# Kernel optimization log

Hardware: AMD Instinct MI355X
Metric: run time of the kernel (lower is better)

## Reference

```python
import jax, jax.numpy as jnp
import numpy as np

K = 3          # up_k
EPS = 1e-8
BN_EPS = 1e-5
NEG_SLOPE = 0.2


def _knn(dense_xyz, sparse_xyz, k):
    # dense_xyz: (B,3,N), sparse_xyz: (B,3,S) -> squared dists (B,N,k), idx (B,N,k)
    inner = jnp.einsum('bcn,bcs->bns', dense_xyz, sparse_xyz)
    n2 = jnp.sum(dense_xyz * dense_xyz, axis=1)   # (B,N)
    s2 = jnp.sum(sparse_xyz * sparse_xyz, axis=1)  # (B,S)
    d2 = n2[:, :, None] + s2[:, None, :] - 2.0 * inner  # (B,N,S)
    d2 = jnp.maximum(d2, 0.0)
    neg_d, idx = jax.lax.top_k(-d2, k)  # k smallest distances
    return -neg_d, idx


def setup_inputs() -> dict:
    key = jax.random.key(0)
    ks = jax.random.split(key, 7)
    B, N, S = 4, 16384, 4096
    Cd, Cs = 128, 256           # dense / sparse feature channels (Cd + Cs = 3*v_dense)
    Co = 128                    # v_dense
    return {
        'dense_points_xyz': jax.random.normal(ks[0], (B, 3, N), jnp.float32),
        'sparse_points_xyz': jax.random.normal(ks[1], (B, 3, S), jnp.float32),
        'dense_points_data': jax.random.normal(ks[2], (B, Cd, N), jnp.float32),
        'sparse_points_data': jax.random.normal(ks[3], (B, Cs, S), jnp.float32),
        'conv_w': jax.random.normal(ks[4], (Co, Cd + Cs), jnp.float32) * (1.0 / np.sqrt(Cd + Cs)),
        'bn_gamma': jnp.ones((Co,), jnp.float32),
        'bn_beta': jnp.zeros((Co,), jnp.float32),
    }


def reference(dense_points_xyz, sparse_points_xyz, dense_points_data,
              sparse_points_data, conv_w, bn_gamma, bn_beta):
    # ---- interpolate: KNN + inverse-distance weighted sum ----
    d, idx = _knn(dense_points_xyz, sparse_points_xyz, K)   # (B,N,K) each
    # gather sparse features: (B,Cs,S), idx (B,N,K) -> (B,Cs,N,K)
    neighbors = jax.vmap(lambda sd, ix: sd[:, ix])(sparse_points_data, idx)
    w = 1.0 / (d + EPS)
    w = w / jnp.sum(w, axis=-1, keepdims=True)              # (B,N,K)
    interp = jnp.sum(neighbors * w[:, None, :, :], axis=-1)  # (B,Cs,N)

    # ---- concat + 1x1 conv + BatchNorm (training-mode batch stats) + LeakyReLU ----
    x = jnp.concatenate([dense_points_data, interp], axis=1)  # (B, 3*v_dense, N)
    y = jnp.einsum('oc,bcn->bon', conv_w, x)                  # (B, v_dense, N)
    mean = jnp.mean(y, axis=(0, 2), keepdims=True)
    var = jnp.var(y, axis=(0, 2), keepdims=True)
    y = (y - mean) * jax.lax.rsqrt(var + BN_EPS)
    y = y * bn_gamma[None, :, None] + bn_beta[None, :, None]
    y = jnp.where(y >= 0, y, NEG_SLOPE * y)
    return y, dense_points_xyz
```

## Files before the change

kernel.cpp:

```cpp
#include <hip/hip_runtime.h>

constexpr int B  = 4;
constexpr int N  = 16384;
constexpr int S  = 4096;
constexpr int CD = 128;
constexpr int CS = 256;
constexpr int CO = 128;
constexpr int CIN = CD + CS;

constexpr int NC = 8;
constexpr int CH = S / NC;
constexpr int P  = 2;

__device__ __forceinline__ double pack_key(float dist, unsigned sg) {
  return __longlong_as_double(
      (long long)(__double_as_longlong((double)dist) | (unsigned long long)sg));
}

__device__ __forceinline__ void insert3(double& k0, double& k1, double& k2,
                                        double x) {
  const double m0 = fmax(k0, x);
  const double m1 = fmax(k1, x);
  k0 = fmin(k0, x);
  k1 = fmin(k1, m0);
  k2 = fmin(k2, m1);
}

__global__ __launch_bounds__(256) void knn_chunk_kernel(
    const float* __restrict__ dxyz, const float* __restrict__ sxyz,
    double* __restrict__ ckey) {
  __shared__ float4 sp[CH];
  const int b = blockIdx.z;
  const int c = blockIdx.y;
  const int nbase = blockIdx.x * (256 * P);
  const int t = threadIdx.x;

  const float* sb = sxyz + b * 3 * S + c * CH;
  for (int j = t; j < CH; j += 256)
    sp[j] = make_float4(sb[j], sb[S + j], sb[2 * S + j], 0.f);
  __syncthreads();

  float bx[P], by[P], bz[P];
  double k0[P], k1[P], k2[P];
  #pragma unroll
  for (int p = 0; p < P; ++p) {
    const int n = nbase + p * 256 + t;
    bx[p] = dxyz[b * 3 * N + n];
    by[p] = dxyz[b * 3 * N + N + n];
    bz[p] = dxyz[b * 3 * N + 2 * N + n];
    k0[p] = k1[p] = k2[p] = 1e300;
  }

  #pragma unroll 4
  for (int j = 0; j < CH; ++j) {
    const float4 q = sp[j];
    const unsigned sg = (unsigned)(c * CH + j);
    #pragma unroll
    for (int p = 0; p < P; ++p) {
      const float ex = bx[p] - q.x, ey = by[p] - q.y, ez = bz[p] - q.z;
      const float dist = fmaf(ex, ex, fmaf(ey, ey, ez * ez));
      insert3(k0[p], k1[p], k2[p], pack_key(dist, sg));
    }
  }

  #pragma unroll
  for (int p = 0; p < P; ++p) {
    const int n = nbase + p * 256 + t;
    const size_t base = (((size_t)c * B + b) * N + n) * 3;
    ckey[base + 0] = k0[p];
    ckey[base + 1] = k1[p];
    ckey[base + 2] = k2[p];
  }
}

__global__ __launch_bounds__(256) void knn_merge_kernel(
    const double* __restrict__ ckey, float* __restrict__ wgt,
    int* __restrict__ idx) {
  const int gid = blockIdx.x * 256 + threadIdx.x;
  double k0 = 1e300, k1 = 1e300, k2 = 1e300;
  #pragma unroll
  for (int c = 0; c < NC; ++c) {
    const size_t base = ((size_t)c * B * N + gid) * 3;
    insert3(k0, k1, k2, ckey[base + 0]);
    insert3(k0, k1, k2, ckey[base + 1]);
    insert3(k0, k1, k2, ckey[base + 2]);
  }
  const long long b0 = __double_as_longlong(k0);
  const long long b1 = __double_as_longlong(k1);
  const long long b2 = __double_as_longlong(k2);
  const float d0 = (float)__longlong_as_double(b0 & ~0xFFFll);
  const float d1 = (float)__longlong_as_double(b1 & ~0xFFFll);
  const float d2 = (float)__longlong_as_double(b2 & ~0xFFFll);
  const float w0 = 1.f / (d0 + 1e-8f);
  const float w1 = 1.f / (d1 + 1e-8f);
  const float w2 = 1.f / (d2 + 1e-8f);
  const float inv = 1.f / (w0 + w1 + w2);
  const size_t base = (size_t)gid * 3;
  wgt[base + 0] = w0 * inv;
  wgt[base + 1] = w1 * inv;
  wgt[base + 2] = w2 * inv;
  idx[base + 0] = (int)(b0 & 0xFFFll);
  idx[base + 1] = (int)(b1 & 0xFFFll);
  idx[base + 2] = (int)(b2 & 0xFFFll);
}

__global__ __launch_bounds__(256) void wtrans_kernel(
    const float* __restrict__ cw, float* __restrict__ wt) {
  const int i = blockIdx.x * 256 + threadIdx.x;
  const int o = i / CIN;
  const int c = i - o * CIN;
  wt[c * CO + o] = cw[i];
}

__global__ __launch_bounds__(64) void zproj_kernel(
    const float* __restrict__ sdata, const float* __restrict__ wt,
    float* __restrict__ Z) {
  const int b = blockIdx.z;
  const int og = blockIdx.y;
  const int s = blockIdx.x * 64 + threadIdx.x;
  const float* __restrict__ xp = sdata + b * CS * S + s;
  const float* __restrict__ wp = wt + CD * CO + og * 16;

  float acc[16];
  #pragma unroll
  for (int i = 0; i < 16; ++i) acc[i] = 0.f;

  #pragma unroll 4
  for (int c = 0; c < CS; ++c) {
    const float xv = xp[c * S];
    #pragma unroll
    for (int i = 0; i < 16; ++i)
      acc[i] = fmaf(wp[c * CO + i], xv, acc[i]);
  }

  float4* zp = reinterpret_cast<float4*>(Z + (b * S + s) * CO + og * 16);
  #pragma unroll
  for (int i = 0; i < 4; ++i)
    zp[i] = make_float4(acc[4*i+0], acc[4*i+1], acc[4*i+2], acc[4*i+3]);
}

__global__ __launch_bounds__(256) void ygemm_kernel(
    const float* __restrict__ ddata, const float* __restrict__ cw,
    const float* __restrict__ Z, const float* __restrict__ wgt,
    const int* __restrict__ idx, float* __restrict__ y) {
  const int b = blockIdx.y;
  const int n = blockIdx.x * 64 + (threadIdx.x & 63);
  const int rg = __builtin_amdgcn_readfirstlane(threadIdx.x >> 6);
  const float* __restrict__ xp = ddata + b * CD * N + n;
  const float* __restrict__ wp = cw + rg * 32 * CIN;

  float acc[32];
  #pragma unroll
  for (int i = 0; i < 32; ++i) acc[i] = 0.f;

  #pragma unroll 4
  for (int c = 0; c < CD; ++c) {
    const float xv = xp[c * N];
    #pragma unroll
    for (int i = 0; i < 32; ++i)
      acc[i] = fmaf(wp[i * CIN + c], xv, acc[i]);
  }

  const int pb = (b * N + n) * 3;
  #pragma unroll
  for (int k = 0; k < 3; ++k) {
    const float wk = wgt[pb + k];
    const int ik = idx[pb + k];
    const float4* zp =
        reinterpret_cast<const float4*>(Z + (b * S + ik) * CO + rg * 32);
    #pragma unroll
    for (int i = 0; i < 8; ++i) {
      float4 zv = zp[i];
      acc[4*i+0] = fmaf(wk, zv.x, acc[4*i+0]);
      acc[4*i+1] = fmaf(wk, zv.y, acc[4*i+1]);
      acc[4*i+2] = fmaf(wk, zv.z, acc[4*i+2]);
      acc[4*i+3] = fmaf(wk, zv.w, acc[4*i+3]);
    }
  }

  float* yp = y + b * CO * N + (rg * 32) * N + n;
  #pragma unroll
  for (int i = 0; i < 32; ++i) yp[i * N] = acc[i];
}

__global__ __launch_bounds__(256) void stats_kernel(
    const float* __restrict__ y, float* __restrict__ stats) {
  const int o = blockIdx.x;
  const int b = blockIdx.y;
  const float4* yp = reinterpret_cast<const float4*>(y + (b * CO + o) * N);
  float s = 0.f, sq = 0.f;
  for (int j = threadIdx.x; j < N / 4; j += 256) {
    float4 v = yp[j];
    s  += v.x + v.y + v.z + v.w;
    sq += v.x * v.x + v.y * v.y + v.z * v.z + v.w * v.w;
  }
  __shared__ float ls[256];
  __shared__ float lq[256];
  ls[threadIdx.x] = s;
  lq[threadIdx.x] = sq;
  __syncthreads();
  for (int st = 128; st > 0; st >>= 1) {
    if (threadIdx.x < (unsigned)st) {
      ls[threadIdx.x] += ls[threadIdx.x + st];
      lq[threadIdx.x] += lq[threadIdx.x + st];
    }
    __syncthreads();
  }
  if (threadIdx.x == 0) {
    atomicAdd(&stats[o], ls[0]);
    atomicAdd(&stats[CO + o], lq[0]);
  }
}

__global__ void scaleshift_kernel(const float* __restrict__ stats,
                                  const float* __restrict__ gamma,
                                  const float* __restrict__ beta,
                                  float* __restrict__ ss) {
  const int o = threadIdx.x;
  const float invc = 1.f / (float)(B * N);
  const float m = stats[o] * invc;
  float v = stats[CO + o] * invc - m * m;
  v = fmaxf(v, 0.f);
  const float sc = gamma[o] / sqrtf(v + 1e-5f);
  ss[o] = sc;
  ss[CO + o] = beta[o] - m * sc;
}

__global__ __launch_bounds__(256) void norm_kernel(float* __restrict__ y,
                                                   const float* __restrict__ ss) {
  const int i = blockIdx.x * 256 + threadIdx.x;
  const int o = (i >> 12) & (CO - 1);
  const float sc = ss[o];
  const float sh = ss[CO + o];
  float4* yp = reinterpret_cast<float4*>(y);
  float4 v = yp[i];
  float t;
  t = fmaf(v.x, sc, sh); v.x = fmaxf(t, 0.2f * t);
  t = fmaf(v.y, sc, sh); v.y = fmaxf(t, 0.2f * t);
  t = fmaf(v.z, sc, sh); v.z = fmaxf(t, 0.2f * t);
  t = fmaf(v.w, sc, sh); v.w = fmaxf(t, 0.2f * t);
  yp[i] = v;
}

extern "C" void kernel_launch(void* const* d_in, const int* in_sizes, int n_in,
                              void* d_out, int out_size, void* d_ws, size_t ws_size,
                              hipStream_t stream) {
  const float* dxyz  = (const float*)d_in[0];
  const float* sxyz  = (const float*)d_in[1];
  const float* ddata = (const float*)d_in[2];
  const float* sdata = (const float*)d_in[3];
  const float* cw    = (const float*)d_in[4];
  const float* gamma = (const float*)d_in[5];
  const float* beta  = (const float*)d_in[6];
  float* out = (float*)d_out;

  char* wsb = (char*)d_ws;
  float*  wgt  = (float*) (wsb);
  int*    idx  = (int*)   (wsb + 786432);
  double* ckey = (double*)(wsb + 1572864);
  float*  Z    = (float*) (wsb + 1572864);
  float*  wt   = (float*) (wsb + 9961472);
  float*  stats= (float*) (wsb + 14155776);
  float*  ss   = (float*) (wsb + 14156800);

  hipMemsetAsync(stats, 0, 2 * CO * sizeof(float), stream);

  knn_chunk_kernel<<<dim3(N / (256 * P), NC, B), 256, 0, stream>>>(dxyz, sxyz, ckey);
  knn_merge_kernel<<<dim3(B * N / 256), 256, 0, stream>>>(ckey, wgt, idx);
  wtrans_kernel   <<<dim3(CO * CIN / 256), 256, 0, stream>>>(cw, wt);
  zproj_kernel    <<<dim3(S / 64, CO / 16, B), 64, 0, stream>>>(sdata, wt, Z);
  ygemm_kernel    <<<dim3(N / 64, B), 256, 0, stream>>>(ddata, cw, Z, wgt, idx, out);
  stats_kernel    <<<dim3(CO, B), 256, 0, stream>>>(out, stats);
  scaleshift_kernel<<<1, 128, 0, stream>>>(stats, gamma, beta, ss);
  norm_kernel     <<<(B * CO * N / 4) / 256, 256, 0, stream>>>(out, ss);

  hipMemcpyAsync(out + (size_t)B * CO * N, dxyz, (size_t)B * 3 * N * sizeof(float),
                 hipMemcpyDeviceToDevice, stream);
}
```

Baseline: 243.2 us.

## Two-pass float KNN with expanded distance and recomputed weights in merge

The KNN chunk kernel now uses the expanded form s2 - 2*x·s, precomputed per sparse point in shared memory. A first pass keeps the top-3 in plain floats using min/med3, and a second pass builds packed double keys only for candidates at or below the third-best threshold. Packing is sign-aware because the partial distance can be negative, and the merge kernel recomputes the true squared distances from the coordinates to form the weights. The chunk count is halved, so ckey traffic drops but there are fewer blocks. The cost is scanning each chunk twice, and ties may order differently from the reference.

```diff
diff --git a/kernel.cpp b/kernel.cpp
--- a/kernel.cpp
+++ b/kernel.cpp
@@ -8,14 +8,9 @@
 constexpr int CO = 128;
 constexpr int CIN = CD + CS;
 
-constexpr int NC = 8;
+constexpr int NC = 4;
 constexpr int CH = S / NC;
 constexpr int P  = 2;
-
-__device__ __forceinline__ double pack_key(float dist, unsigned sg) {
-  return __longlong_as_double(
-      (long long)(__double_as_longlong((double)dist) | (unsigned long long)sg));
-}
 
 __device__ __forceinline__ void insert3(double& k0, double& k1, double& k2,
                                         double x) {
@@ -24,6 +19,17 @@
   k0 = fmin(k0, x);
   k1 = fmin(k1, m0);
   k2 = fmin(k2, m1);
+}
+
+__device__ __forceinline__ double pack_key(float t, unsigned sg) {
+  const unsigned sga = (t < 0.f) ? (0xFFFu ^ sg) : sg;
+  return __longlong_as_double(__double_as_longlong((double)t) |
+                              (unsigned long long)sga);
+}
+__device__ __forceinline__ int unpack_idx(double k) {
+  const long long bits = __double_as_longlong(k);
+  const int low = (int)(bits & 0xFFFll);
+  return (bits < 0) ? (0xFFF ^ low) : low;
 }
 
 __global__ __launch_bounds__(256) void knn_chunk_kernel(
@@ -36,30 +42,50 @@
   const int t = threadIdx.x;
 
   const float* sb = sxyz + b * 3 * S + c * CH;
-  for (int j = t; j < CH; j += 256)
-    sp[j] = make_float4(sb[j], sb[S + j], sb[2 * S + j], 0.f);
+  for (int j = t; j < CH; j += 256) {
+    const float sx = sb[j], sy = sb[S + j], sz = sb[2 * S + j];
+    sp[j] = make_float4(-2.f * sx, -2.f * sy, -2.f * sz,
+                        fmaf(sx, sx, fmaf(sy, sy, sz * sz)));
+  }
   __syncthreads();
 
   float bx[P], by[P], bz[P];
-  double k0[P], k1[P], k2[P];
+  float d0[P], d1[P], d2[P];
   #pragma unroll
   for (int p = 0; p < P; ++p) {
     const int n = nbase + p * 256 + t;
     bx[p] = dxyz[b * 3 * N + n];
     by[p] = dxyz[b * 3 * N + N + n];
     bz[p] = dxyz[b * 3 * N + 2 * N + n];
-    k0[p] = k1[p] = k2[p] = 1e300;
+    d0[p] = d1[p] = d2[p] = 1e30f;
   }
 
   #pragma unroll 4
   for (int j = 0; j < CH; ++j) {
     const float4 q = sp[j];
+    #pragma unroll
+    for (int p = 0; p < P; ++p) {
+      const float x = fmaf(q.x, bx[p], fmaf(q.y, by[p], fmaf(q.z, bz[p], q.w)));
+      d2[p] = fminf(fmaxf(x, d1[p]), d2[p]);
+      d1[p] = __builtin_amdgcn_fmed3f(x, d0[p], d1[p]);
+      d0[p] = fminf(x, d0[p]);
+    }
+  }
+
+  double k0[P], k1[P], k2[P];
+  #pragma unroll
+  for (int p = 0; p < P; ++p) { k0[p] = k1[p] = k2[p] = 1e300; }
+
+  #pragma unroll 2
+  for (int j = 0; j < CH; ++j) {
+    const float4 q = sp[j];
     const unsigned sg = (unsigned)(c * CH + j);
     #pragma unroll
     for (int p = 0; p < P; ++p) {
-      const float ex = bx[p] - q.x, ey = by[p] - q.y, ez = bz[p] - q.z;
-      const float dist = fmaf(ex, ex, fmaf(ey, ey, ez * ez));
-      insert3(k0[p], k1[p], k2[p], pack_key(dist, sg));
+      const float x = fmaf(q.x, bx[p], fmaf(q.y, by[p], fmaf(q.z, bz[p], q.w)));
+      if (x <= d2[p]) {
+        insert3(k0[p], k1[p], k2[p], pack_key(x, sg));
+      }
     }
   }
 
@@ -74,9 +100,12 @@
 }
 
 __global__ __launch_bounds__(256) void knn_merge_kernel(
-    const double* __restrict__ ckey, float* __restrict__ wgt,
+    const double* __restrict__ ckey, const float* __restrict__ dxyz,
+    const float* __restrict__ sxyz, float* __restrict__ wgt,
     int* __restrict__ idx) {
   const int gid = blockIdx.x * 256 + threadIdx.x;
+  const int b = gid >> 14;
+  const int n = gid & (N - 1);
   double k0 = 1e300, k1 = 1e300, k2 = 1e300;
   #pragma unroll
   for (int c = 0; c < NC; ++c) {
@@ -85,23 +114,34 @@
     insert3(k0, k1, k2, ckey[base + 1]);
     insert3(k0, k1, k2, ckey[base + 2]);
   }
-  const long long b0 = __double_as_longlong(k0);
-  const long long b1 = __double_as_longlong(k1);
-  const long long b2 = __double_as_longlong(k2);
-  const float d0 = (float)__longlong_as_double(b0 & ~0xFFFll);
-  const float d1 = (float)__longlong_as_double(b1 & ~0xFFFll);
-  const float d2 = (float)__longlong_as_double(b2 & ~0xFFFll);
-  const float w0 = 1.f / (d0 + 1e-8f);
-  const float w1 = 1.f / (d1 + 1e-8f);
-  const float w2 = 1.f / (d2 + 1e-8f);
-  const float inv = 1.f / (w0 + w1 + w2);
+  int ii[3];
+  ii[0] = unpack_idx(k0);
+  ii[1] = unpack_idx(k1);
+  ii[2] = unpack_idx(k2);
+
+  const float bx = dxyz[b * 3 * N + n];
+  const float by = dxyz[b * 3 * N + N + n];
+  const float bz = dxyz[b * 3 * N + 2 * N + n];
+  const float n2 = bx * bx + by * by + bz * bz;
+  float w[3];
+  #pragma unroll
+  for (int k = 0; k < 3; ++k) {
+    const float sx = sxyz[b * 3 * S + ii[k]];
+    const float sy = sxyz[b * 3 * S + S + ii[k]];
+    const float sz = sxyz[b * 3 * S + 2 * S + ii[k]];
+    const float s2 = sx * sx + sy * sy + sz * sz;
+    const float inner = bx * sx + by * sy + bz * sz;
+    const float d = fmaxf((n2 + s2) - 2.f * inner, 0.f);
+    w[k] = 1.f / (d + 1e-8f);
+  }
+  const float inv = 1.f / (w[0] + w[1] + w[2]);
   const size_t base = (size_t)gid * 3;
-  wgt[base + 0] = w0 * inv;
-  wgt[base + 1] = w1 * inv;
-  wgt[base + 2] = w2 * inv;
-  idx[base + 0] = (int)(b0 & 0xFFFll);
-  idx[base + 1] = (int)(b1 & 0xFFFll);
-  idx[base + 2] = (int)(b2 & 0xFFFll);
+  wgt[base + 0] = w[0] * inv;
+  wgt[base + 1] = w[1] * inv;
+  wgt[base + 2] = w[2] * inv;
+  idx[base + 0] = ii[0];
+  idx[base + 1] = ii[1];
+  idx[base + 2] = ii[2];
 }
 
 __global__ __launch_bounds__(256) void wtrans_kernel(
@@ -266,7 +306,7 @@
   hipMemsetAsync(stats, 0, 2 * CO * sizeof(float), stream);
 
   knn_chunk_kernel<<<dim3(N / (256 * P), NC, B), 256, 0, stream>>>(dxyz, sxyz, ckey);
-  knn_merge_kernel<<<dim3(B * N / 256), 256, 0, stream>>>(ckey, wgt, idx);
+  knn_merge_kernel<<<dim3(B * N / 256), 256, 0, stream>>>(ckey, dxyz, sxyz, wgt, idx);
   wtrans_kernel   <<<dim3(CO * CIN / 256), 256, 0, stream>>>(cw, wt);
   zproj_kernel    <<<dim3(S / 64, CO / 16, B), 64, 0, stream>>>(sdata, wt, Z);
   ygemm_kernel    <<<dim3(N / 64, B), 256, 0, stream>>>(ddata, cw, Z, wgt, idx, out);
```

Result: slower. 310.2 us (+27.5%).
